# Kernel tuning notes

Hardware: AMD Instinct MI355X
Metric: run time of the kernel (lower is better)

The kernel has to match this reference:

```python
import jax, jax.numpy as jnp
import numpy as np

HEADS = 2


def _log_cpb(h, w, w1, b1, w2):
    # Swin-v2 style continuous relative position bias on an h*w grid.
    yy, xx = jnp.meshgrid(jnp.arange(h), jnp.arange(w), indexing='ij')
    coords = jnp.stack([yy.reshape(-1), xx.reshape(-1)], axis=-1).astype(jnp.float32)  # (L, 2)
    rel = coords[:, None, :] - coords[None, :, :]                                      # (L, L, 2)
    denom = jnp.array([max(h - 1, 1), max(w - 1, 1)], dtype=jnp.float32)
    rel = rel / denom * 8.0
    rel = jnp.sign(rel) * jnp.log2(1.0 + jnp.abs(rel)) / np.float32(np.log2(8.0))
    bias = jax.nn.relu(rel @ w1.T + b1) @ w2.T                                         # (L, L, heads)
    return jnp.transpose(bias, (2, 0, 1))                                              # (heads, L, L)


def setup_inputs() -> dict:
    key = jax.random.key(0)
    ks = jax.random.split(key, 11)
    b, s, c, h, w = 2, 32, 128, 24, 24
    hid, out_ch = 256, 128
    sc = lambda n: 1.0 / np.sqrt(n)
    return {
        'x':      jax.random.normal(ks[0], (b, s, c, h, w), jnp.float32),
        'qk_w':   jax.random.normal(ks[1], (2 * c, c), jnp.float32) * sc(c),
        'v_w':    jax.random.normal(ks[2], (hid, c), jnp.float32) * sc(c),
        'cpb_w1': jax.random.normal(ks[3], (c, 2), jnp.float32) * sc(2),
        'cpb_b1': jax.random.normal(ks[4], (c,), jnp.float32) * 0.02,
        'cpb_w2': jax.random.normal(ks[5], (HEADS, c), jnp.float32) * sc(c),
        'sa_bias': jax.random.uniform(ks[6], (hid, 1, 1), jnp.float32, -sc(c), sc(c)),
        'mlp_w1': jax.random.normal(ks[7], (hid, hid), jnp.float32) * sc(hid),
        'mlp_b1': jax.random.normal(ks[8], (hid,), jnp.float32) * 0.02,
        'mlp_w2': jax.random.normal(ks[9], (out_ch, hid), jnp.float32) * sc(hid),
        'mlp_b2': jax.random.normal(ks[10], (out_ch,), jnp.float32) * 0.02,
    }


def reference(x, qk_w, v_w, cpb_w1, cpb_b1, cpb_w2, sa_bias, mlp_w1, mlp_b1, mlp_w2, mlp_b2):
    b, s, c, h, w = x.shape
    L = h * w
    qkd = c // HEADS
    vd = v_w.shape[0] // HEADS
    xr = x.reshape(b * s, c, L)                                        # flatten (b s) and (h w)
    # QKV via 1x1 convs == channel matmuls
    qk = jnp.einsum('oc,bcl->bol', qk_w, xr)                           # (bs, 2c, L)
    qk = qk.reshape(b * s, 2, HEADS, qkd, L).transpose(1, 0, 2, 4, 3)  # (2, bs, heads, L, d)
    q, k = qk[0], qk[1]
    v = jnp.einsum('oc,bcl->bol', v_w, xr).reshape(b * s, HEADS, vd, L).transpose(0, 1, 3, 2)
    # learned continuous relative position bias, added as SDPA attn_mask
    bias = _log_cpb(h, w, cpb_w1, cpb_b1, cpb_w2)                      # (heads, L, L)
    scale = np.float32(1.0 / np.sqrt(qkd))
    scores = jnp.einsum('bhld,bhmd->bhlm', q, k) * scale + bias[None]
    attn = jax.nn.softmax(scores, axis=-1)
    out = jnp.einsum('bhlm,bhmd->bhld', attn, v)                       # (bs, heads, L, vd)
    out = out.transpose(0, 1, 3, 2).reshape(b, s, HEADS * vd, h, w)
    out = out + sa_bias[None, None]                                    # (b, s, hid, h, w)
    # 1x1-conv MLP with exact GELU
    y = jnp.einsum('oi,bsihw->bsohw', mlp_w1, out) + mlp_b1[None, None, :, None, None]
    y = jax.nn.gelu(y, approximate=False)
    y = jnp.einsum('oi,bsihw->bsohw', mlp_w2, y) + mlp_b2[None, None, :, None, None]
    return y
```

## Files before the change

kernel.cpp:

```cpp
#include <hip/hip_runtime.h>
#include <cstdint>
#include <cstddef>

constexpr int BS   = 64;
constexpr int Cc   = 128;
constexpr int Lc   = 576;
constexpr int VD   = 128;
constexpr int HID  = 256;
constexpr int OUTC = 128;
constexpr int NPIX = BS * Lc;

typedef __bf16 bf16x8 __attribute__((ext_vector_type(8)));
typedef float  f32x4  __attribute__((ext_vector_type(4)));
typedef unsigned short u16x8 __attribute__((ext_vector_type(8)));
typedef unsigned int   u32x4 __attribute__((ext_vector_type(4)));

__device__ __forceinline__ unsigned short f2bf(float f) {
  unsigned int u = __builtin_bit_cast(unsigned int, f);
  u += 0x7fffu + ((u >> 16) & 1u);
  return (unsigned short)(u >> 16);
}
__device__ __forceinline__ float bf2f(unsigned short h) {
  unsigned int u = ((unsigned int)h) << 16;
  return __builtin_bit_cast(float, u);
}
__device__ __forceinline__ unsigned int packhl(float v) {
  unsigned short hi = f2bf(v);
  unsigned short lo = f2bf(v - bf2f(hi));
  return ((unsigned int)hi << 16) | (unsigned int)lo;
}
__device__ __forceinline__ void unpack8(u32x4 a, u32x4 b, bf16x8& hi, bf16x8& lo) {
  u32x4 h, l;
  h[0] = (a[1] & 0xffff0000u) | (a[0] >> 16);
  l[0] = (a[1] << 16)         | (a[0] & 0xffffu);
  h[1] = (a[3] & 0xffff0000u) | (a[2] >> 16);
  l[1] = (a[3] << 16)         | (a[2] & 0xffffu);
  h[2] = (b[1] & 0xffff0000u) | (b[0] >> 16);
  l[2] = (b[1] << 16)         | (b[0] & 0xffffu);
  h[3] = (b[3] & 0xffff0000u) | (b[2] >> 16);
  l[3] = (b[3] << 16)         | (b[2] & 0xffffu);
  hi = __builtin_bit_cast(bf16x8, h);
  lo = __builtin_bit_cast(bf16x8, l);
}

#define MFMA16(a, b, c) __builtin_amdgcn_mfma_f32_16x16x32_bf16((a), (b), (c), 0, 0, 0)

__global__ __launch_bounds__(256) void cpb_kernel(const float* __restrict__ w1,
                                                  const float* __restrict__ b1,
                                                  const float* __restrict__ w2,
                                                  float* __restrict__ tab) {
  int idx = blockIdx.x * 256 + threadIdx.x;
  if (idx >= 47 * 47) return;
  int dy = idx / 47 - 23, dx = idx % 47 - 23;
  float fy = (float)dy * (8.0f / 23.0f);
  float fx = (float)dx * (8.0f / 23.0f);
  fy = copysignf(log2f(1.0f + fabsf(fy)) * (1.0f / 3.0f), fy);
  fx = copysignf(log2f(1.0f + fabsf(fx)) * (1.0f / 3.0f), fx);
  float a0 = 0.f, a1 = 0.f;
  for (int hh = 0; hh < 128; hh++) {
    float hv = fmaxf(w1[2 * hh] * fy + w1[2 * hh + 1] * fx + b1[hh], 0.f);
    a0 += w2[hh] * hv;
    a1 += w2[128 + hh] * hv;
  }
  tab[idx] = a0;
  tab[2209 + idx] = a1;
}

__global__ __launch_bounds__(256) void bias_mat(const float* __restrict__ tab,
                                                unsigned short* __restrict__ biasC) {
  int id = blockIdx.x * 256 + threadIdx.x;
  if (id >= 737280) return;
  int id2 = id % 2560;
  int grp = id / 2560;
  int wave = grp & 3;
  int mt = (grp >> 2) % 36;
  int hh = grp / 144;
  int g = id2 / 512;
  int lane = (id2 >> 3) & 63;
  int k = id2 & 7;
  int e = g * 8 + k;
  unsigned short val = 0;
  if (e < 36) {
    int ln = e >> 2, r = e & 3;
    int nt = wave * 9 + ln;
    int i = mt * 16 + (lane >> 4) * 4 + r;
    int j = nt * 16 + (lane & 15);
    int yi = i / 24, xi = i - yi * 24;
    int yj = j / 24, xj = j - yj * 24;
    val = f2bf(tab[hh * 2209 + (yi - yj + 23) * 47 + (xi - xj + 23)]);
  }
  biasC[id] = val;
}

__global__ __launch_bounds__(256) void prep_w(
    const float* __restrict__ w1, const float* __restrict__ w2,
    const float* __restrict__ qkw, const float* __restrict__ vw,
    unsigned short* __restrict__ w1h, unsigned short* __restrict__ w1l,
    unsigned short* __restrict__ w2h, unsigned short* __restrict__ w2l,
    unsigned short* __restrict__ wqkh, unsigned short* __restrict__ wqkl,
    unsigned short* __restrict__ wvh, unsigned short* __restrict__ wvl) {
  int id = blockIdx.x * 256 + threadIdx.x;
  const float* src;
  unsigned short *dh, *dl;
  int off;
  if (id < 65536)       { src = w1;  dh = w1h;  dl = w1l;  off = id; }
  else if (id < 98304)  { src = w2;  dh = w2h;  dl = w2l;  off = id - 65536; }
  else if (id < 131072) { src = qkw; dh = wqkh; dl = wqkl; off = id - 98304; }
  else if (id < 163840) { src = vw;  dh = wvh;  dl = wvl;  off = id - 131072; }
  else return;
  float v = src[off];
  unsigned short hi = f2bf(v);
  dh[off] = hi;
  dl[off] = f2bf(v - bf2f(hi));
}

__global__ __launch_bounds__(256) void prep_x(const float* __restrict__ x,
                                              unsigned short* __restrict__ xph,
                                              unsigned short* __restrict__ xpl) {
  __shared__ float xt[128 * 65];
  const int l0 = blockIdx.x * 64, bs = blockIdx.y;
  const int t = threadIdx.x;
  const float* xb = x + (size_t)bs * Cc * Lc;
#pragma unroll
  for (int pass = 0; pass < 8; pass++) {
    int f = pass * 1024 + t * 4;
    int c = f >> 6, ll = f & 63;
    *(float4*)(xt + c * 65 + ll) = *(const float4*)(xb + c * Lc + l0 + ll);
  }
  __syncthreads();
  const int rowl = t >> 2, c0 = (t & 3) * 32;
  const size_t p = (size_t)bs * Lc + l0 + rowl;
  unsigned short hbuf[32], lbuf[32];
#pragma unroll
  for (int i = 0; i < 32; i++) {
    float v = xt[(c0 + i) * 65 + rowl];
    unsigned short hi = f2bf(v);
    hbuf[i] = hi;
    lbuf[i] = f2bf(v - bf2f(hi));
  }
#pragma unroll
  for (int g = 0; g < 4; g++) {
    *(u16x8*)(xph + p * 128 + c0 + g * 8) = *(u16x8*)(hbuf + g * 8);
    *(u16x8*)(xpl + p * 128 + c0 + g * 8) = *(u16x8*)(lbuf + g * 8);
  }
}

__global__ __launch_bounds__(256, 2) void qkv_mfma(
    const unsigned short* __restrict__ xh, const unsigned short* __restrict__ xl,
    const unsigned short* __restrict__ wqkh, const unsigned short* __restrict__ wqkl,
    const unsigned short* __restrict__ wvh, const unsigned short* __restrict__ wvl,
    unsigned short* __restrict__ qg, unsigned short* __restrict__ kg,
    unsigned short* __restrict__ vg) {
  __shared__ unsigned short vt[128 * 130];
  const int t = threadIdx.x;
  const int wv = t >> 6, lane = t & 63;
  const int quad = lane >> 4, cc = lane & 15;
  const int by = blockIdx.y;
  const int n0 = (wv >> 1) * 64;
  const unsigned short* Wh = (by < 2) ? wqkh : wvh;
  const unsigned short* Wl = (by < 2) ? wqkl : wvl;
  const int wrow0 = (by & 1) * 128 + n0;
  f32x4 acc[4][4];
#pragma unroll
  for (int i = 0; i < 4; i++)
#pragma unroll
    for (int j = 0; j < 4; j++) acc[i][j] = (f32x4){0.f, 0.f, 0.f, 0.f};
  {
    const int srow = lane >> 3;
    const int schunk = (lane & 7) ^ srow;
    const size_t grow = (size_t)(blockIdx.x * 128 + wv * 32 + srow) * 128;
    const unsigned short* asrc = (schunk < 4)
                                     ? (xh + grow + (schunk << 3))
                                     : (xl + grow + ((schunk - 4) << 3));
    unsigned short* adst = vt + wv * 2048;
#pragma unroll
    for (int s = 0; s < 4; s++)
      __builtin_amdgcn_global_load_lds(
          (const __attribute__((address_space(1))) unsigned int*)(asrc + s * 1024),
          (__attribute__((address_space(3))) unsigned int*)(adst + s * 512),
          16, 0, 0);
    for (int kc = 0; kc < 4; kc++) {
      __syncthreads();
      const int bufo = (kc & 1) << 13;
      bf16x8 Ah[4], Al[4], Bh[4], Bl[4];
#pragma unroll
      for (int i = 0; i < 4; i++) {
        const int row = (wv & 1) * 64 + i * 16 + cc;
        const unsigned short* ab = vt + bufo + row * 64;
        Ah[i] = *(const bf16x8*)(ab + ((quad ^ (cc & 7)) << 3));
        Al[i] = *(const bf16x8*)(ab + (((quad + 4) ^ (cc & 7)) << 3));
      }
      if (kc < 3) {
        const int nb = ((kc + 1) & 1) << 13;
#pragma unroll
        for (int s = 0; s < 4; s++)
          __builtin_amdgcn_global_load_lds(
              (const __attribute__((address_space(1))) unsigned int*)(
                  asrc + (kc + 1) * 32 + s * 1024),
              (__attribute__((address_space(3))) unsigned int*)(adst + nb +
                                                                s * 512),
              16, 0, 0);
      }
      const int kb = kc * 32 + quad * 8;
#pragma unroll
      for (int i = 0; i < 4; i++) {
        size_t br = (size_t)(wrow0 + i * 16 + cc) * 128 + kb;
        Bh[i] = *(const bf16x8*)(Wh + br);
        Bl[i] = *(const bf16x8*)(Wl + br);
      }
#pragma unroll
      for (int i = 0; i < 4; i++)
#pragma unroll
        for (int j = 0; j < 4; j++) {
          acc[i][j] = MFMA16(Ah[i], Bh[j], acc[i][j]);
          acc[i][j] = MFMA16(Al[i], Bh[j], acc[i][j]);
          acc[i][j] = MFMA16(Ah[i], Bl[j], acc[i][j]);
        }
    }
  }
  __syncthreads();
  if (by < 2) {
    const float sc = (by == 0) ? 0.125f : 1.0f;
#pragma unroll
    for (int j = 0; j < 4; j++) {
      int o = n0 + j * 16 + cc;
#pragma unroll
      for (int i = 0; i < 4; i++)
#pragma unroll
        for (int r = 0; r < 4; r++) {
          int pl = (wv & 1) * 64 + i * 16 + quad * 4 + r;
          vt[pl * 130 + o] = f2bf(acc[i][j][r] * sc);
        }
    }
    __syncthreads();
    unsigned short* dst = (by == 0) ? qg : kg;
    const int pl = t >> 1, head = t & 1;
    const int p = blockIdx.x * 128 + pl;
    const int bs = p / 576, l = p - bs * 576;
    unsigned short* drow = dst + ((size_t)(bs * 2 + head) * Lc + l) * 64;
#pragma unroll
    for (int g = 0; g < 8; g++)
      *(u16x8*)(drow + g * 8) = *(const u16x8*)(vt + pl * 130 + head * 64 + g * 8);
  } else {
    const int head = by - 2;
#pragma unroll
    for (int j = 0; j < 4; j++) {
      int d = n0 + j * 16 + cc;
#pragma unroll
      for (int i = 0; i < 4; i++)
#pragma unroll
        for (int r = 0; r < 4; r++) {
          int pl = (wv & 1) * 64 + i * 16 + quad * 4 + r;
          vt[d * 130 + pl] = f2bf(acc[i][j][r]);
        }
    }
    __syncthreads();
    const int d = t >> 1, half = (t & 1) * 64;
#pragma unroll
    for (int c8 = 0; c8 < 8; c8++) {
      int pl = half + c8 * 8;
      int p = blockIdx.x * 128 + pl;
      int bs = p / 576, l = p - bs * 576;
      *(u16x8*)(vg + ((size_t)(bs * 2 + head) * VD + d) * Lc + l) =
          *(u16x8*)(vt + d * 130 + pl);
    }
  }
}

__global__ __launch_bounds__(256, 4) void attn_kernel(
    const unsigned short* __restrict__ qg,
    const unsigned short* __restrict__ kg,
    const unsigned short* __restrict__ vg,
    const unsigned short* __restrict__ biasC,
    const float* __restrict__ sa_bias,
    unsigned int* __restrict__ aout_p) {
  constexpr int PP = 580;
  __shared__ unsigned short Pb[32 * PP];
  __shared__ float psum[4][32];
  const int f = blockIdx.x;
  const int g = f >> 3;
  const int pair = (f & 7) + 8 * (g / 18);
  const int bm = g % 18;
  const int hh = pair & 1, bs = pair >> 1;
  const int m0 = bm * 32;
  const int t = threadIdx.x;
  const int wv = t >> 6, lane = t & 63;
  const int quad = lane >> 4, c = lane & 15;
  const int c7 = c & 7;
  const unsigned short* qb = qg + ((size_t)pair * Lc + m0) * 64;
  const unsigned short* kb = kg + (size_t)pair * Lc * 64;
  const unsigned short* vb = vg + (size_t)pair * VD * Lc;
  bf16x8 qa0[2], qa1[2];
#pragma unroll
  for (int mt = 0; mt < 2; mt++) {
    const unsigned short* qp = qb + (size_t)(mt * 16 + c) * 64 + quad * 8;
    qa0[mt] = *(const bf16x8*)qp;
    qa1[mt] = *(const bf16x8*)(qp + 32);
  }
  f32x4 S[2][9];
#pragma unroll
  for (int mt = 0; mt < 2; mt++) {
    const unsigned short* bbase =
        biasC + ((((size_t)hh * 36 + (bm * 2 + mt)) * 4 + wv) * 5) * 512;
#pragma unroll
    for (int g2 = 0; g2 < 5; g2++) {
      u16x8 bv = *(const u16x8*)(bbase + g2 * 512 + lane * 8);
#pragma unroll
      for (int k = 0; k < 8; k++) {
        int e = g2 * 8 + k;
        if (e < 36) S[mt][e >> 2][e & 3] = bf2f(bv[k]);
      }
    }
  }
  {
    unsigned short* Ks = Pb + wv * 1024;
    const int srow = lane >> 3;
    const unsigned short* ksrc = kb + (size_t)(wv * 144 + srow) * 64 +
                                 (((lane & 7) ^ srow) << 3);
#pragma unroll
    for (int tt = 0; tt < 2; tt++)
#pragma unroll
      for (int s = 0; s < 2; s++)
        __builtin_amdgcn_global_load_lds(
            (const __attribute__((address_space(1))) unsigned int*)(
                ksrc + tt * 1024 + s * 512),
            (__attribute__((address_space(3))) unsigned int*)(
                Ks + tt * 4096 + s * 512),
            16, 0, 0);
#pragma unroll
    for (int ln = 0; ln < 9; ln++) {
      if (ln + 2 < 9) {
        asm volatile("s_waitcnt lgkmcnt(0)" ::: "memory");
        __builtin_amdgcn_sched_barrier(0);
#pragma unroll
        for (int s = 0; s < 2; s++)
          __builtin_amdgcn_global_load_lds(
              (const __attribute__((address_space(1))) unsigned int*)(
                  ksrc + (ln + 2) * 1024 + s * 512),
              (__attribute__((address_space(3))) unsigned int*)(
                  Ks + ((ln + 2) % 3) * 4096 + s * 512),
              16, 0, 0);
        asm volatile("s_waitcnt vmcnt(4)" ::: "memory");
      } else if (ln == 7) {
        asm volatile("s_waitcnt vmcnt(2)" ::: "memory");
      } else {
        asm volatile("s_waitcnt vmcnt(0)" ::: "memory");
      }
      __builtin_amdgcn_sched_barrier(0);
      const unsigned short* kbuf = Ks + (ln % 3) * 4096;
      bf16x8 b0 = *(const bf16x8*)(kbuf + c * 64 + ((quad ^ c7) << 3));
      bf16x8 b1 = *(const bf16x8*)(kbuf + c * 64 + (((quad + 4) ^ c7) << 3));
#pragma unroll
      for (int mt = 0; mt < 2; mt++)
        S[mt][ln] = MFMA16(qa1[mt], b1, MFMA16(qa0[mt], b0, S[mt][ln]));
    }
  }
  __syncthreads();
  float sm[2][4] = {{0.f, 0.f, 0.f, 0.f}, {0.f, 0.f, 0.f, 0.f}};
#pragma unroll
  for (int mt = 0; mt < 2; mt++)
#pragma unroll
    for (int ln = 0; ln < 9; ln++)
#pragma unroll
      for (int r = 0; r < 4; r++) {
        float e = __expf(S[mt][ln][r]);
        sm[mt][r] += e;
        Pb[(mt * 16 + quad * 4 + r) * PP + (wv * 9 + ln) * 16 + c] = f2bf(e);
      }
#pragma unroll
  for (int sh = 1; sh < 16; sh <<= 1)
#pragma unroll
    for (int mt = 0; mt < 2; mt++)
#pragma unroll
      for (int r = 0; r < 4; r++) sm[mt][r] += __shfl_xor(sm[mt][r], sh);
  if (c == 0)
#pragma unroll
    for (int mt = 0; mt < 2; mt++)
#pragma unroll
      for (int r = 0; r < 4; r++)
        psum[wv][mt * 16 + quad * 4 + r] = sm[mt][r];
  __syncthreads();
  float inv[2][4];
#pragma unroll
  for (int mt = 0; mt < 2; mt++)
#pragma unroll
    for (int r = 0; r < 4; r++) {
      int row = mt * 16 + quad * 4 + r;
      inv[mt][r] =
          1.0f / (psum[0][row] + psum[1][row] + psum[2][row] + psum[3][row]);
    }
  const int nd0 = wv * 2;
  f32x4 O[2][2];
#pragma unroll
  for (int mt = 0; mt < 2; mt++)
#pragma unroll
    for (int dd = 0; dd < 2; dd++) O[mt][dd] = (f32x4){0.f, 0.f, 0.f, 0.f};
#pragma unroll
  for (int kc = 0; kc < 18; kc++) {
    bf16x8 pa[2];
#pragma unroll
    for (int mt = 0; mt < 2; mt++)
      pa[mt] = *(const bf16x8*)(Pb + (size_t)(mt * 16 + c) * PP + kc * 32 +
                                quad * 8);
#pragma unroll
    for (int dd = 0; dd < 2; dd++) {
      bf16x8 vf = *(const bf16x8*)(vb + (size_t)((nd0 + dd) * 16 + c) * Lc +
                                   kc * 32 + quad * 8);
#pragma unroll
      for (int mt = 0; mt < 2; mt++) O[mt][dd] = MFMA16(pa[mt], vf, O[mt][dd]);
    }
  }
  unsigned int* obp = aout_p + ((size_t)bs * Lc + m0) * HID + hh * 128;
#pragma unroll
  for (int dd = 0; dd < 2; dd++) {
    float sb = sa_bias[hh * 128 + (nd0 + dd) * 16 + c];
#pragma unroll
    for (int mt = 0; mt < 2; mt++)
#pragma unroll
      for (int r = 0; r < 4; r++) {
        float v = O[mt][dd][r] * inv[mt][r] + sb;
        obp[(size_t)(mt * 16 + quad * 4 + r) * HID + (nd0 + dd) * 16 + c] =
            packhl(v);
      }
  }
}

__global__ __launch_bounds__(256, 4) void mlp_fused(
    const unsigned int* __restrict__ ap,
    const unsigned short* __restrict__ w1h, const unsigned short* __restrict__ w1l,
    const float* __restrict__ b1,
    const unsigned short* __restrict__ w2h, const unsigned short* __restrict__ w2l,
    const float* __restrict__ b2, float* __restrict__ out) {
  constexpr int YPW = 260;
  __shared__ unsigned int lds[32 * YPW];
  const int t = threadIdx.x;
  const int wv = t >> 6, lane = t & 63;
  const int quad = lane >> 4, cc = lane & 15;
  const int c7 = cc & 7;
  const int M0 = blockIdx.x * 32;

  const unsigned int* gsrc = ap + (size_t)(M0 + 8 * wv + (lane >> 3)) * HID +
                             (((lane & 7) ^ (lane >> 3)) << 2);
  __builtin_amdgcn_global_load_lds(
      (const __attribute__((address_space(1))) unsigned int*)gsrc,
      (__attribute__((address_space(3))) unsigned int*)(&lds[wv * 256]),
      16, 0, 0);

  const int n0 = wv * 64;
  f32x4 acc1[2][4];
#pragma unroll
  for (int i = 0; i < 2; i++)
#pragma unroll
    for (int j = 0; j < 4; j++) acc1[i][j] = (f32x4){0.f, 0.f, 0.f, 0.f};
  for (int kc = 0; kc < 8; kc++) {
    __syncthreads();
    const int bufw = (kc & 1) << 10;
    bf16x8 Ah[2], Al[2];
#pragma unroll
    for (int i = 0; i < 2; i++) {
      const int row = i * 16 + cc;
      u32x4 pa = *(const u32x4*)&lds[bufw + row * 32 + (((2 * quad) ^ c7) << 2)];
      u32x4 pb =
          *(const u32x4*)&lds[bufw + row * 32 + (((2 * quad + 1) ^ c7) << 2)];
      unpack8(pa, pb, Ah[i], Al[i]);
    }
    if (kc < 7) {
      __builtin_amdgcn_global_load_lds(
          (const __attribute__((address_space(1))) unsigned int*)(gsrc +
                                                                  (kc + 1) * 32),
          (__attribute__((address_space(3))) unsigned int*)(
              &lds[(((kc + 1) & 1) << 10) + wv * 256]),
          16, 0, 0);
    }
    const int kb = kc * 32 + quad * 8;
    bf16x8 Bh[4], Bl[4];
#pragma unroll
    for (int j = 0; j < 4; j++) {
      size_t br = (size_t)(n0 + j * 16 + cc) * HID + kb;
      Bh[j] = *(const bf16x8*)(w1h + br);
      Bl[j] = *(const bf16x8*)(w1l + br);
    }
#pragma unroll
    for (int i = 0; i < 2; i++)
#pragma unroll
      for (int j = 0; j < 4; j++) {
        acc1[i][j] = MFMA16(Ah[i], Bh[j], acc1[i][j]);
        acc1[i][j] = MFMA16(Al[i], Bh[j], acc1[i][j]);
        acc1[i][j] = MFMA16(Ah[i], Bl[j], acc1[i][j]);
      }
  }
  __syncthreads();
#pragma unroll
  for (int j = 0; j < 4; j++) {
    int col = n0 + j * 16 + cc;
    float bias = b1[col];
#pragma unroll
    for (int i = 0; i < 2; i++)
#pragma unroll
      for (int r = 0; r < 4; r++) {
        int row = i * 16 + quad * 4 + r;
        float v = acc1[i][j][r] + bias;
        float g = 0.5f * v * (1.0f + erff(v * 0.70710678118654752f));
        lds[row * YPW + col] = packhl(g);
      }
  }
  __syncthreads();
  {
    const int n2 = wv * 32;
    f32x4 acc2[2][2];
#pragma unroll
    for (int i = 0; i < 2; i++)
#pragma unroll
      for (int j = 0; j < 2; j++) acc2[i][j] = (f32x4){0.f, 0.f, 0.f, 0.f};
    for (int kc = 0; kc < 8; kc++) {
      const int kb = kc * 32 + quad * 8;
      bf16x8 Ah[2], Al[2], Bh[2], Bl[2];
#pragma unroll
      for (int i = 0; i < 2; i++) {
        const unsigned int* arow = &lds[(i * 16 + cc) * YPW + kb];
        u32x4 pa = *(const u32x4*)arow;
        u32x4 pb = *(const u32x4*)(arow + 4);
        unpack8(pa, pb, Ah[i], Al[i]);
      }
#pragma unroll
      for (int j = 0; j < 2; j++) {
        size_t br = (size_t)(n2 + j * 16 + cc) * HID + kb;
        Bh[j] = *(const bf16x8*)(w2h + br);
        Bl[j] = *(const bf16x8*)(w2l + br);
      }
#pragma unroll
      for (int i = 0; i < 2; i++)
#pragma unroll
        for (int j = 0; j < 2; j++) {
          acc2[i][j] = MFMA16(Ah[i], Bh[j], acc2[i][j]);
          acc2[i][j] = MFMA16(Al[i], Bh[j], acc2[i][j]);
          acc2[i][j] = MFMA16(Ah[i], Bl[j], acc2[i][j]);
        }
    }
#pragma unroll
    for (int i = 0; i < 2; i++) {
      int p = M0 + i * 16 + quad * 4;
      int bs = p / Lc, l = p - bs * Lc;
#pragma unroll
      for (int j = 0; j < 2; j++) {
        int col = n2 + j * 16 + cc;
        float bias = b2[col];
        float4 v = make_float4(acc2[i][j][0] + bias, acc2[i][j][1] + bias,
                               acc2[i][j][2] + bias, acc2[i][j][3] + bias);
        *(float4*)(out + ((size_t)bs * OUTC + col) * Lc + l) = v;
      }
    }
  }
}

extern "C" void kernel_launch(void* const* d_in, const int* in_sizes, int n_in,
                              void* d_out, int out_size, void* d_ws, size_t ws_size,
                              hipStream_t stream) {
  const float* x    = (const float*)d_in[0];
  const float* qk_w = (const float*)d_in[1];
  const float* v_w  = (const float*)d_in[2];
  const float* cw1  = (const float*)d_in[3];
  const float* cb1  = (const float*)d_in[4];
  const float* cw2  = (const float*)d_in[5];
  const float* sab  = (const float*)d_in[6];
  const float* mw1  = (const float*)d_in[7];
  const float* mb1  = (const float*)d_in[8];
  const float* mw2  = (const float*)d_in[9];
  const float* mb2  = (const float*)d_in[10];
  float* out = (float*)d_out;
  char* ws = (char*)d_ws;

  float* tab = (float*)(ws);
  unsigned short* biasC  = (unsigned short*)(ws + 65536);
  unsigned short* qg     = (unsigned short*)(ws + 1572864);
  unsigned short* kg     = (unsigned short*)(ws + 11010048);
  unsigned short* vg     = (unsigned short*)(ws + 20447232);
  unsigned short* xph    = (unsigned short*)(ws + 39321600);
  unsigned short* xpl    = (unsigned short*)(ws + 48758784);
  unsigned int*   aout_p = (unsigned int*)(ws + 58195968);
  unsigned short* w1h    = (unsigned short*)(ws + 95944704);
  unsigned short* w1l    = (unsigned short*)(ws + 96075776);
  unsigned short* w2h    = (unsigned short*)(ws + 96206848);
  unsigned short* w2l    = (unsigned short*)(ws + 96272384);
  unsigned short* wqkh   = (unsigned short*)(ws + 96337920);
  unsigned short* wqkl   = (unsigned short*)(ws + 96403456);
  unsigned short* wvh    = (unsigned short*)(ws + 96468992);
  unsigned short* wvl    = (unsigned short*)(ws + 96534528);

  cpb_kernel<<<dim3(9), dim3(256), 0, stream>>>(cw1, cb1, cw2, tab);
  bias_mat<<<dim3(2880), dim3(256), 0, stream>>>(tab, biasC);
  prep_w<<<dim3(640), dim3(256), 0, stream>>>(mw1, mw2, qk_w, v_w,
                                              w1h, w1l, w2h, w2l,
                                              wqkh, wqkl, wvh, wvl);
  prep_x<<<dim3(9, 64), dim3(256), 0, stream>>>(x, xph, xpl);
  qkv_mfma<<<dim3(288, 4), dim3(256), 0, stream>>>(xph, xpl, wqkh, wqkl,
                                                   wvh, wvl, qg, kg, vg);
  attn_kernel<<<dim3(2304), dim3(256), 0, stream>>>(qg, kg, vg, biasC, sab,
                                                    aout_p);
  mlp_fused<<<dim3(1152), dim3(256), 0, stream>>>(aout_p, w1h, w1l, mb1,
                                                  w2h, w2l, mb2, out);
}
```

Measured before the change: 260.2 us.

## Prefetch all MLP input chunks to LDS up front with staged vmcnt waits

The MLP kernel now issues all eight async global-to-LDS loads for its 32-row activation tile at kernel start instead of double-buffering one chunk per iteration. Each k-step waits with a graded s_waitcnt vmcnt and a barrier, and the loop is fully unrolled. The LDS buffer shrinks to 8192 words with an XOR-swizzled layout for the GELU intermediate, replacing the padded row stride, and launch bounds are raised to 5 blocks per CU. This aims to hide global latency and raise occupancy, at the cost of relying on precise vmcnt ordering and extra register pressure from unrolling.

```diff
diff --git a/kernel.cpp b/kernel.cpp
--- a/kernel.cpp
+++ b/kernel.cpp
@@ -425,14 +425,13 @@
   }
 }
 
-__global__ __launch_bounds__(256, 4) void mlp_fused(
+__global__ __launch_bounds__(256, 5) void mlp_fused(
     const unsigned int* __restrict__ ap,
     const unsigned short* __restrict__ w1h, const unsigned short* __restrict__ w1l,
     const float* __restrict__ b1,
     const unsigned short* __restrict__ w2h, const unsigned short* __restrict__ w2l,
     const float* __restrict__ b2, float* __restrict__ out) {
-  constexpr int YPW = 260;
-  __shared__ unsigned int lds[32 * YPW];
+  __shared__ unsigned int lds[8192];
   const int t = threadIdx.x;
   const int wv = t >> 6, lane = t & 63;
   const int quad = lane >> 4, cc = lane & 15;
@@ -441,10 +440,13 @@
 
   const unsigned int* gsrc = ap + (size_t)(M0 + 8 * wv + (lane >> 3)) * HID +
                              (((lane & 7) ^ (lane >> 3)) << 2);
-  __builtin_amdgcn_global_load_lds(
-      (const __attribute__((address_space(1))) unsigned int*)gsrc,
-      (__attribute__((address_space(3))) unsigned int*)(&lds[wv * 256]),
-      16, 0, 0);
+#pragma unroll
+  for (int s = 0; s < 8; s++)
+    __builtin_amdgcn_global_load_lds(
+        (const __attribute__((address_space(1))) unsigned int*)(gsrc + s * 32),
+        (__attribute__((address_space(3))) unsigned int*)(
+            &lds[s * 1024 + wv * 256]),
+        16, 0, 0);
 
   const int n0 = wv * 64;
   f32x4 acc1[2][4];
@@ -452,9 +454,19 @@
   for (int i = 0; i < 2; i++)
 #pragma unroll
     for (int j = 0; j < 4; j++) acc1[i][j] = (f32x4){0.f, 0.f, 0.f, 0.f};
+#pragma unroll
   for (int kc = 0; kc < 8; kc++) {
-    __syncthreads();
-    const int bufw = (kc & 1) << 10;
+    if (kc == 0)      asm volatile("s_waitcnt vmcnt(7)" ::: "memory");
+    else if (kc == 1) asm volatile("s_waitcnt vmcnt(6)" ::: "memory");
+    else if (kc == 2) asm volatile("s_waitcnt vmcnt(5)" ::: "memory");
+    else if (kc == 3) asm volatile("s_waitcnt vmcnt(4)" ::: "memory");
+    else if (kc == 4) asm volatile("s_waitcnt vmcnt(3)" ::: "memory");
+    else if (kc == 5) asm volatile("s_waitcnt vmcnt(2)" ::: "memory");
+    else if (kc == 6) asm volatile("s_waitcnt vmcnt(1)" ::: "memory");
+    else              asm volatile("s_waitcnt vmcnt(0)" ::: "memory");
+    __builtin_amdgcn_s_barrier();
+    __builtin_amdgcn_sched_barrier(0);
+    const int bufw = kc << 10;
     bf16x8 Ah[2], Al[2];
 #pragma unroll
     for (int i = 0; i < 2; i++) {
@@ -464,14 +476,6 @@
           *(const u32x4*)&lds[bufw + row * 32 + (((2 * quad + 1) ^ c7) << 2)];
       unpack8(pa, pb, Ah[i], Al[i]);
     }
-    if (kc < 7) {
-      __builtin_amdgcn_global_load_lds(
-          (const __attribute__((address_space(1))) unsigned int*)(gsrc +
-                                                                  (kc + 1) * 32),
-          (__attribute__((address_space(3))) unsigned int*)(
-              &lds[(((kc + 1) & 1) << 10) + wv * 256]),
-          16, 0, 0);
-    }
     const int kb = kc * 32 + quad * 8;
     bf16x8 Bh[4], Bl[4];
 #pragma unroll
@@ -501,7 +505,8 @@
         int row = i * 16 + quad * 4 + r;
         float v = acc1[i][j][r] + bias;
         float g = 0.5f * v * (1.0f + erff(v * 0.70710678118654752f));
-        lds[row * YPW + col] = packhl(g);
+        lds[row * 256 + ((((col >> 2) ^ (row & 7)) << 2) | (col & 3))] =
+            packhl(g);
       }
   }
   __syncthreads();
@@ -517,9 +522,11 @@
       bf16x8 Ah[2], Al[2], Bh[2], Bl[2];
 #pragma unroll
       for (int i = 0; i < 2; i++) {
-        const unsigned int* arow = &lds[(i * 16 + cc) * YPW + kb];
-        u32x4 pa = *(const u32x4*)arow;
-        u32x4 pb = *(const u32x4*)(arow + 4);
+        const int row = i * 16 + cc;
+        const int r7 = row & 7;
+        const unsigned int* base = lds + row * 256;
+        u32x4 pa = *(const u32x4*)(base + ((((kb >> 2)) ^ r7) << 2));
+        u32x4 pb = *(const u32x4*)(base + ((((kb >> 2) + 1) ^ r7) << 2));
         unpack8(pa, pb, Ah[i], Al[i]);
       }
 #pragma unroll
```

Result: slower. 267.9 us (+3.0%).
